# Kernel tuning notes

Hardware: AMD Instinct MI355X
Metric: run time of the kernel (lower is better)

The kernel has to match this reference:

```python
import jax, jax.numpy as jnp
import numpy as np

B = 16          # scene pairs
SRC_N = 512     # src nodes per pair (constant in this setup; reference handles ragged)
REF_N = 512
N_SRC = B * SRC_N
N_REF = B * REF_N
N_TOT = N_SRC + N_REF   # 16384 objects total
P = 128                 # points per object
FEAT = 256              # SGNet node-feature dim / output dim
EMB = 100               # emb_dim
PT_OUT = 256            # pt_out_dim


def setup_inputs() -> dict:
    key = jax.random.key(0)
    ks = jax.random.split(key, 20)
    s = lambda k, *sh: jax.random.normal(k, sh, dtype=jnp.float32) * 0.05
    inp = {
        'tot_obj_pts': jax.random.normal(ks[0], (N_TOT, P, 3), dtype=jnp.float32),
        'src_node_feat': jax.random.normal(ks[1], (N_SRC, FEAT), dtype=jnp.float32),
        'ref_node_feat': jax.random.normal(ks[2], (N_REF, FEAT), dtype=jnp.float32),
        'graph_per_obj_count': jnp.full((B, 2), SRC_N, dtype=jnp.int64),
        'overlap': jax.random.uniform(ks[3], (B,), dtype=jnp.float32),
        'target': jax.random.randint(ks[4], (N_TOT,), 0, 2, dtype=jnp.int64),
        # SGNet (per-node MLP 256 -> 256 -> 256)
        'sg_w1': s(ks[5], FEAT, FEAT), 'sg_b1': jnp.zeros((FEAT,), jnp.float32),
        'sg_w2': s(ks[6], FEAT, FEAT), 'sg_b2': jnp.zeros((FEAT,), jnp.float32),
        # structure_embedding Linear(256, 100)
        'se_w': s(ks[7], FEAT, EMB), 'se_b': jnp.zeros((EMB,), jnp.float32),
        # PointNetfeat 1x1 convs: 3 -> 64 -> 128 -> 256, global max pool
        'p_w1': s(ks[8], 3, 64),    'p_b1': jnp.zeros((64,), jnp.float32),
        'p_w2': s(ks[9], 64, 128),  'p_b2': jnp.zeros((128,), jnp.float32),
        'p_w3': s(ks[10], 128, PT_OUT), 'p_b3': jnp.zeros((PT_OUT,), jnp.float32),
        # object_embedding Linear(256, 100)
        'oe_w': s(ks[11], PT_OUT, EMB), 'oe_b': jnp.zeros((EMB,), jnp.float32),
    }
    return inp


def _interleave_positions(counts):
    """Output positions reproducing the per-pair cat([src_i, ref_i]) ordering."""
    src_c = counts[:, 0]
    ref_c = counts[:, 1]
    excl = lambda c: jnp.concatenate([jnp.zeros((1,), c.dtype), jnp.cumsum(c)[:-1]])
    src_starts = excl(src_c)
    ref_starts = excl(ref_c)
    out_starts = excl(src_c + ref_c)
    b = counts.shape[0]
    b_src = jnp.repeat(jnp.arange(b), src_c, total_repeat_length=N_SRC)
    b_ref = jnp.repeat(jnp.arange(b), ref_c, total_repeat_length=N_REF)
    pos_src = out_starts[b_src] + (jnp.arange(N_SRC) - src_starts[b_src])
    pos_ref = out_starts[b_ref] + src_c[b_ref] + (jnp.arange(N_REF) - ref_starts[b_ref])
    return pos_src, pos_ref


def reference(tot_obj_pts, src_node_feat, ref_node_feat, graph_per_obj_count,
              overlap, target, sg_w1, sg_b1, sg_w2, sg_b2, se_w, se_b,
              p_w1, p_b1, p_w2, p_b2, p_w3, p_b3, oe_w, oe_b):
    # ---- sgnet branch: per-node MLP, then ragged interleave per scene pair ----
    sgnet = lambda x: jax.nn.relu(x @ sg_w1 + sg_b1) @ sg_w2 + sg_b2
    src_emb = sgnet(src_node_feat)   # [N_SRC, 256]
    ref_emb = sgnet(ref_node_feat)   # [N_REF, 256]
    pos_src, pos_ref = _interleave_positions(graph_per_obj_count)
    structure = jnp.zeros((N_TOT, FEAT), src_emb.dtype)
    structure = structure.at[pos_src].set(src_emb).at[pos_ref].set(ref_emb)
    sg_out = structure @ se_w + se_b          # [N_TOT, 100]

    # ---- point branch: PointNet 1x1-conv stack + global max pool ----
    # tot_obj_pts.permute(0,2,1): [N, P, 3] -> per-point linears via einsum
    h = jax.nn.relu(jnp.einsum('npc,cd->npd', tot_obj_pts, p_w1) + p_b1)
    h = jax.nn.relu(jnp.einsum('npc,cd->npd', h, p_w2) + p_b2)
    h = jnp.einsum('npc,cd->npd', h, p_w3) + p_b3   # [N, P, 256]
    feat = jnp.max(h, axis=1)                        # global max over points
    pt_out = feat @ oe_w + oe_b                      # [N_TOT, 100]

    # ---- joint embedding: cat along feature dim ----
    joint = jnp.concatenate([sg_out, pt_out], axis=1)  # [N_TOT, 200]
    return joint
```

## Files before the change

### kernel.cpp

```cpp
#include <hip/hip_runtime.h>
#include <hip/hip_bf16.h>
#include <math.h>

#define B_SZ   16
#define SRC_N  512
#define N_TOT  16384
#define P_PTS  128
#define FEAT   256
#define EMB    100
#define OUT_C  200

typedef __attribute__((ext_vector_type(8))) short short8;
typedef __attribute__((ext_vector_type(8))) unsigned short ushort8;
typedef __attribute__((ext_vector_type(4))) float floatx4;

__device__ __forceinline__ unsigned short f2bf(float x) {
    union { float f; unsigned u; } v; v.f = x;
    unsigned r = v.u + 0x7fffu + ((v.u >> 16) & 1u);
    return (unsigned short)(r >> 16);
}
__device__ __forceinline__ unsigned pack_rne(float a, float b) {
    union { float f; unsigned u; } x, y; x.f = a; y.f = b;
    unsigned lo = x.u + 0x7fffu + ((x.u >> 16) & 1u);
    unsigned hi = y.u + 0x7fffu + ((y.u >> 16) & 1u);
    return __builtin_amdgcn_perm(hi, lo, 0x07060302);
}
__device__ __forceinline__ unsigned pack_rhu(float a, float b) {
    union { float f; unsigned u; } x, y; x.f = a; y.f = b;
    return __builtin_amdgcn_perm(y.u + 0x8000u, x.u + 0x8000u, 0x07060302);
}

#define WS_PW2T 0
#define WS_PW3T 8192
#define WS_POET 40960
#define WS_SGW1 66560
#define WS_SGW2 132096
#define WS_SGSE 197632
#define WS_TOT  226304

__device__ __forceinline__ int perm32(int p) {
    return 32 * (p >> 5) + 16 * (p & 1) + ((p >> 1) & 15);
}

__global__ void prep_kernel(const float* __restrict__ pw2,
                            const float* __restrict__ pw3,
                            const float* __restrict__ oew,
                            const float* __restrict__ sw1,
                            const float* __restrict__ sw2,
                            const float* __restrict__ sew,
                            unsigned short* __restrict__ ws) {
    const int o = blockIdx.x * 256 + threadIdx.x;
    if (o < WS_PW3T) {
        const int n = o >> 6, k = o & 63;
        ws[o] = f2bf(pw2[k * 128 + n]);
    } else if (o < WS_POET) {
        const int i = o - WS_PW3T;
        const int n = i >> 7, k = i & 127;
        ws[o] = f2bf(pw3[k * 256 + n]);
    } else if (o < WS_SGW1) {
        const int i = o - WS_POET;
        const int j = i >> 8, c = i & 255;
        ws[o] = f2bf(oew[c * EMB + j]);
    } else if (o < WS_SGW2) {
        const int i = o - WS_SGW1;
        const int n = i >> 8, k = i & 255;
        ws[o] = f2bf(sw1[k * 256 + n]);
    } else if (o < WS_SGSE) {
        const int i = o - WS_SGW2;
        const int n = i >> 8, kp = i & 255;
        ws[o] = f2bf(sw2[perm32(kp) * 256 + n]);
    } else if (o < WS_TOT) {
        const int i = o - WS_SGSE;
        const int n = i >> 8, kp = i & 255;
        ws[o] = (n < EMB) ? f2bf(sew[perm32(kp) * EMB + n]) : (unsigned short)0;
    }
}

#define SXS 264

template <bool RELU>
__device__ __forceinline__ void sg_layer(const unsigned short* s_in,
                                         unsigned short* s_out,
                                         const unsigned short* wT,
                                         const float* __restrict__ bias,
                                         int wave, int lm, int lq) {
#pragma unroll
    for (int np = 0; np < 2; np++) {
        short8 bf[2][8];
        float bv[2];
#pragma unroll
        for (int b = 0; b < 2; b++) {
            const int n = wave * 64 + (2 * np + b) * 16 + lm;
            bv[b] = bias[n];
#pragma unroll
            for (int kc = 0; kc < 8; kc++)
                bf[b][kc] = *(const short8*)&wT[n * 256 + kc * 32 + lq * 8];
        }
        floatx4 acc[2][2];
#pragma unroll
        for (int b = 0; b < 2; b++)
#pragma unroll
            for (int mt = 0; mt < 2; mt++) acc[b][mt] = {0.f, 0.f, 0.f, 0.f};
#pragma unroll
        for (int mt = 0; mt < 2; mt++) {
            short8 af[8];
#pragma unroll
            for (int kc = 0; kc < 8; kc++)
                af[kc] = *(const short8*)&s_in[(mt * 16 + lm) * SXS + kc * 32 + lq * 8];
#pragma unroll
            for (int b = 0; b < 2; b++)
#pragma unroll
                for (int kc = 0; kc < 8; kc++)
                    acc[b][mt] = __builtin_amdgcn_mfma_f32_16x16x32_bf16(
                        af[kc], bf[b][kc], acc[b][mt], 0, 0, 0);
        }
#pragma unroll
        for (int mt = 0; mt < 2; mt++)
#pragma unroll
            for (int r = 0; r < 4; r++) {
                float v0 = acc[0][mt][r] + bv[0];
                float v1 = acc[1][mt][r] + bv[1];
                if (RELU) { v0 = fmaxf(v0, 0.f); v1 = fmaxf(v1, 0.f); }
                *(unsigned*)&s_out[(mt * 16 + lq * 4 + r) * SXS +
                                   wave * 64 + 32 * np + 2 * lm] = pack_rne(v0, v1);
            }
    }
}

__global__ __launch_bounds__(256, 2) void sgnet_mfma_kernel(
    const float* __restrict__ src_feat, const float* __restrict__ ref_feat,
    const float* __restrict__ b1, const float* __restrict__ b2,
    const float* __restrict__ seb, const unsigned short* __restrict__ ws,
    float* __restrict__ out)
{
    __shared__ __align__(16) unsigned short s_x[32 * SXS];
    __shared__ __align__(16) unsigned short s_h[32 * SXS];

    const unsigned short* w1T = ws + WS_SGW1;
    const unsigned short* w2T = ws + WS_SGW2;
    const unsigned short* seT = ws + WS_SGSE;

    const int blk = blockIdx.x;
    const bool is_ref = (blk >= 256);
    const int row0 = (blk & 255) * 32;
    const float* feat = is_ref ? ref_feat : src_feat;
    const int t = threadIdx.x;
    const int wave = t >> 6, lane = t & 63, lm = lane & 15, lq = lane >> 4;

#pragma unroll
    for (int i = 0; i < 4; i++) {
        const int flat = i * 2048 + t * 8;
        const int r = flat >> 8, c = flat & 255;
        const float4 a = *(const float4*)&feat[(row0 + r) * 256 + c];
        const float4 b = *(const float4*)&feat[(row0 + r) * 256 + c + 4];
        uint4 d;
        d.x = pack_rne(a.x, a.y); d.y = pack_rne(a.z, a.w);
        d.z = pack_rne(b.x, b.y); d.w = pack_rne(b.z, b.w);
        *(uint4*)&s_x[r * SXS + c] = d;
    }
    __syncthreads();

    sg_layer<true>(s_x, s_h, w1T, b1, wave, lm, lq);
    __syncthreads();
    sg_layer<false>(s_h, s_x, w2T, b2, wave, lm, lq);
    __syncthreads();

#pragma unroll
    for (int s = 0; s < 2; s++) {
        const int ntt = wave * 2 + s;
        if (ntt >= 7) continue;
        const int j = ntt * 16 + lm;
        short8 bf[8];
#pragma unroll
        for (int kc = 0; kc < 8; kc++)
            bf[kc] = *(const short8*)&seT[j * 256 + kc * 32 + lq * 8];
        const float bj = (j < EMB) ? seb[j] : 0.f;
#pragma unroll
        for (int mt = 0; mt < 2; mt++) {
            short8 af[8];
#pragma unroll
            for (int kc = 0; kc < 8; kc++)
                af[kc] = *(const short8*)&s_x[(mt * 16 + lm) * SXS + kc * 32 + lq * 8];
            floatx4 acc = {0.f, 0.f, 0.f, 0.f};
#pragma unroll
            for (int kc = 0; kc < 8; kc++)
                acc = __builtin_amdgcn_mfma_f32_16x16x32_bf16(af[kc], bf[kc], acc, 0, 0, 0);
            if (j < EMB) {
#pragma unroll
                for (int r = 0; r < 4; r++) {
                    const int grow = row0 + mt * 16 + lq * 4 + r;
                    const int pos = ((grow >> 9) << 10) + (grow & 511) + (is_ref ? 512 : 0);
                    out[pos * OUT_C + j] = acc[r] + bj;
                }
            }
        }
    }
}

#define H1S 72
#define H2S 136

__global__ __launch_bounds__(256, 3) void pointnet_mfma_kernel(
    const float* __restrict__ pts,
    const float* __restrict__ w1, const float* __restrict__ b1,
    const float* __restrict__ b2, const float* __restrict__ b3,
    const unsigned short* __restrict__ ws,
    const float* __restrict__ oeb, float* __restrict__ out)
{
    __shared__ __align__(16) unsigned short s_h1[128 * H1S];
    __shared__ __align__(16) unsigned short s_h2[128 * H2S];
    float* s_pts  = (float*)s_h2;
    float* s_tmp  = (float*)s_h1;
    float* s_feat = (float*)s_h1 + 16 * 264;

    const unsigned short* w2T = ws + WS_PW2T;
    const unsigned short* w3T = ws + WS_PW3T;
    const unsigned short* oeT = ws + WS_POET;

    const int obj  = blockIdx.x;
    const int t    = threadIdx.x;
    const int wave = t >> 6, lane = t & 63, lm = lane & 15, lq = lane >> 4;

    short8 w2f[2][2];
    float4 b2v[2];
#pragma unroll
    for (int mi = 0; mi < 2; mi++) {
        const int m = (wave * 2 + mi) * 16 + lm;
#pragma unroll
        for (int kc = 0; kc < 2; kc++)
            w2f[mi][kc] = *(const short8*)&w2T[m * 64 + kc * 32 + lq * 8];
        b2v[mi] = *(const float4*)&b2[(wave * 2 + mi) * 16 + lq * 4];
    }

    for (int i = t; i < P_PTS * 3; i += 256)
        s_pts[i] = pts[obj * (P_PTS * 3) + i];
    __syncthreads();

    {
        const int k0 = (t & 7) * 8;
        float wr0[8], wr1[8], wr2[8], br[8];
#pragma unroll
        for (int j = 0; j < 8; j++) {
            wr0[j] = w1[k0 + j]; wr1[j] = w1[64 + k0 + j];
            wr2[j] = w1[128 + k0 + j]; br[j] = b1[k0 + j];
        }
#pragma unroll
        for (int i = 0; i < 4; i++) {
            const int m = (t >> 3) + i * 32;
            const float x = s_pts[m * 3 + 0];
            const float y = s_pts[m * 3 + 1];
            const float z = s_pts[m * 3 + 2];
            float v[8];
#pragma unroll
            for (int j = 0; j < 8; j++)
                v[j] = fmaxf(br[j] + x * wr0[j] + y * wr1[j] + z * wr2[j], 0.f);
            uint4 d;
            d.x = pack_rhu(v[0], v[1]); d.y = pack_rhu(v[2], v[3]);
            d.z = pack_rhu(v[4], v[5]); d.w = pack_rhu(v[6], v[7]);
            *(uint4*)&s_h1[m * H1S + k0] = d;
        }
    }

    short8 w3f[4][4];
#pragma unroll
    for (int mi = 0; mi < 4; mi++) {
        const int m = (wave * 4 + mi) * 16 + lm;
#pragma unroll
        for (int kc = 0; kc < 4; kc++)
            w3f[mi][kc] = *(const short8*)&w3T[m * 128 + kc * 32 + lq * 8];
    }
    __syncthreads();

#pragma unroll
    for (int nt = 0; nt < 8; nt++) {
        short8 hf[2];
#pragma unroll
        for (int kc = 0; kc < 2; kc++)
            hf[kc] = *(const short8*)&s_h1[(nt * 16 + lm) * H1S + kc * 32 + lq * 8];
#pragma unroll
        for (int mi = 0; mi < 2; mi++) {
            floatx4 acc = {0.f, 0.f, 0.f, 0.f};
            acc = __builtin_amdgcn_mfma_f32_16x16x32_bf16(w2f[mi][0], hf[0], acc, 0, 0, 0);
            acc = __builtin_amdgcn_mfma_f32_16x16x32_bf16(w2f[mi][1], hf[1], acc, 0, 0, 0);
            const float v0 = fmaxf(acc[0] + b2v[mi].x, 0.f);
            const float v1 = fmaxf(acc[1] + b2v[mi].y, 0.f);
            const float v2 = fmaxf(acc[2] + b2v[mi].z, 0.f);
            const float v3 = fmaxf(acc[3] + b2v[mi].w, 0.f);
            uint2 dd;
            dd.x = pack_rhu(v0, v1);
            dd.y = pack_rhu(v2, v3);
            *(uint2*)&s_h2[(nt * 16 + lm) * H2S + (wave * 2 + mi) * 16 + lq * 4] = dd;
        }
    }
    __syncthreads();

    {
        floatx4 mx[4];
#pragma unroll
        for (int mi = 0; mi < 4; mi++) mx[mi] = {-1e30f, -1e30f, -1e30f, -1e30f};
#pragma unroll
        for (int nt = 0; nt < 8; nt++) {
            short8 hf[4];
#pragma unroll
            for (int kc = 0; kc < 4; kc++)
                hf[kc] = *(const short8*)&s_h2[(nt * 16 + lm) * H2S + kc * 32 + lq * 8];
#pragma unroll
            for (int mi = 0; mi < 4; mi++) {
                floatx4 acc = {0.f, 0.f, 0.f, 0.f};
#pragma unroll
                for (int kc = 0; kc < 4; kc++)
                    acc = __builtin_amdgcn_mfma_f32_16x16x32_bf16(w3f[mi][kc], hf[kc], acc, 0, 0, 0);
#pragma unroll
                for (int r = 0; r < 4; r++)
                    mx[mi][r] = fmaxf(mx[mi][r], acc[r]);
            }
        }
#pragma unroll
        for (int mi = 0; mi < 4; mi++)
            *(floatx4*)&s_tmp[lm * 264 + (wave * 4 + mi) * 16 + lq * 4] = mx[mi];
    }
    __syncthreads();

    {
        float m = s_tmp[t];
#pragma unroll
        for (int l = 1; l < 16; l++) m = fmaxf(m, s_tmp[l * 264 + t]);
        s_feat[t] = m + b3[t];
    }
    __syncthreads();

    if (t < 2 * EMB) {
        const int j = t >> 1, half = t & 1;
        float acc = half ? 0.f : oeb[j];
        const unsigned short* orow = &oeT[j * 256 + half * 128];
        const float* f = &s_feat[half * 128];
        for (int c8 = 0; c8 < 16; c8++) {
            const ushort8 w8 = *(const ushort8*)&orow[c8 * 8];
            const float4 f0 = *(const float4*)&f[c8 * 8];
            const float4 f1 = *(const float4*)&f[c8 * 8 + 4];
            union { unsigned u; float fl; } cv;
            float s = 0.f;
            cv.u = (unsigned)w8[0] << 16; s += f0.x * cv.fl;
            cv.u = (unsigned)w8[1] << 16; s += f0.y * cv.fl;
            cv.u = (unsigned)w8[2] << 16; s += f0.z * cv.fl;
            cv.u = (unsigned)w8[3] << 16; s += f0.w * cv.fl;
            cv.u = (unsigned)w8[4] << 16; s += f1.x * cv.fl;
            cv.u = (unsigned)w8[5] << 16; s += f1.y * cv.fl;
            cv.u = (unsigned)w8[6] << 16; s += f1.z * cv.fl;
            cv.u = (unsigned)w8[7] << 16; s += f1.w * cv.fl;
            acc += s;
        }
        acc += __shfl_xor(acc, 1, 64);
        if (half == 0) out[obj * OUT_C + EMB + j] = acc;
    }
}

extern "C" void kernel_launch(void* const* d_in, const int* in_sizes, int n_in,
                              void* d_out, int out_size, void* d_ws, size_t ws_size,
                              hipStream_t stream) {
    (void)in_sizes; (void)n_in; (void)out_size; (void)ws_size;
    const float* tot_pts  = (const float*)d_in[0];
    const float* src_feat = (const float*)d_in[1];
    const float* ref_feat = (const float*)d_in[2];
    const float* sg_w1 = (const float*)d_in[6];
    const float* sg_b1 = (const float*)d_in[7];
    const float* sg_w2 = (const float*)d_in[8];
    const float* sg_b2 = (const float*)d_in[9];
    const float* se_w  = (const float*)d_in[10];
    const float* se_b  = (const float*)d_in[11];
    const float* p_w1  = (const float*)d_in[12];
    const float* p_b1  = (const float*)d_in[13];
    const float* p_w2  = (const float*)d_in[14];
    const float* p_b2  = (const float*)d_in[15];
    const float* p_w3  = (const float*)d_in[16];
    const float* p_b3  = (const float*)d_in[17];
    const float* oe_w  = (const float*)d_in[18];
    const float* oe_b  = (const float*)d_in[19];
    float* out = (float*)d_out;
    unsigned short* ws = (unsigned short*)d_ws;

    prep_kernel<<<(WS_TOT + 255) / 256, 256, 0, stream>>>(
        p_w2, p_w3, oe_w, sg_w1, sg_w2, se_w, ws);
    sgnet_mfma_kernel<<<512, 256, 0, stream>>>(src_feat, ref_feat, sg_b1, sg_b2,
                                               se_b, ws, out);
    pointnet_mfma_kernel<<<N_TOT, 256, 0, stream>>>(tot_pts, p_w1, p_b1,
                                                    p_b2, p_b3, ws, oe_b, out);
}
```

Baseline: 416.2 us.

## Fuse SGNet and PointNet into one launch and halve PointNet h2 buffer

```diff
diff --git a/kernel.cpp b/kernel.cpp
--- a/kernel.cpp
+++ b/kernel.cpp
@@ -77,6 +77,9 @@
 }
 
 #define SXS 264
+#define H1S 72
+#define H2S 136
+#define SMEM_BYTES 35840
 
 template <bool RELU>
 __device__ __forceinline__ void sg_layer(const unsigned short* s_in,
@@ -127,20 +130,22 @@
     }
 }
 
-__global__ __launch_bounds__(256, 2) void sgnet_mfma_kernel(
-    const float* __restrict__ src_feat, const float* __restrict__ ref_feat,
-    const float* __restrict__ b1, const float* __restrict__ b2,
-    const float* __restrict__ seb, const unsigned short* __restrict__ ws,
-    float* __restrict__ out)
+__device__ void sgnet_body(unsigned char* smem, int blk,
+                           const float* __restrict__ src_feat,
+                           const float* __restrict__ ref_feat,
+                           const float* __restrict__ b1,
+                           const float* __restrict__ b2,
+                           const float* __restrict__ seb,
+                           const unsigned short* __restrict__ ws,
+                           float* __restrict__ out)
 {
-    __shared__ __align__(16) unsigned short s_x[32 * SXS];
-    __shared__ __align__(16) unsigned short s_h[32 * SXS];
+    unsigned short* s_x = (unsigned short*)smem;
+    unsigned short* s_h = s_x + 32 * SXS;
 
     const unsigned short* w1T = ws + WS_SGW1;
     const unsigned short* w2T = ws + WS_SGW2;
     const unsigned short* seT = ws + WS_SGSE;
 
-    const int blk = blockIdx.x;
     const bool is_ref = (blk >= 256);
     const int row0 = (blk & 255) * 32;
     const float* feat = is_ref ? ref_feat : src_feat;
@@ -197,18 +202,18 @@
     }
 }
 
-#define H1S 72
-#define H2S 136
-
-__global__ __launch_bounds__(256, 3) void pointnet_mfma_kernel(
-    const float* __restrict__ pts,
-    const float* __restrict__ w1, const float* __restrict__ b1,
-    const float* __restrict__ b2, const float* __restrict__ b3,
-    const unsigned short* __restrict__ ws,
-    const float* __restrict__ oeb, float* __restrict__ out)
+__device__ void pointnet_body(unsigned char* smem, int obj,
+                              const float* __restrict__ pts,
+                              const float* __restrict__ w1,
+                              const float* __restrict__ b1,
+                              const float* __restrict__ b2,
+                              const float* __restrict__ b3,
+                              const unsigned short* __restrict__ ws,
+                              const float* __restrict__ oeb,
+                              float* __restrict__ out)
 {
-    __shared__ __align__(16) unsigned short s_h1[128 * H1S];
-    __shared__ __align__(16) unsigned short s_h2[128 * H2S];
+    unsigned short* s_h1 = (unsigned short*)smem;
+    unsigned short* s_h2 = (unsigned short*)(smem + 18432);
     float* s_pts  = (float*)s_h2;
     float* s_tmp  = (float*)s_h1;
     float* s_feat = (float*)s_h1 + 16 * 264;
@@ -217,8 +222,7 @@
     const unsigned short* w3T = ws + WS_PW3T;
     const unsigned short* oeT = ws + WS_POET;
 
-    const int obj  = blockIdx.x;
-    const int t    = threadIdx.x;
+    const int t = threadIdx.x;
     const int wave = t >> 6, lane = t & 63, lm = lane & 15, lq = lane >> 4;
 
     short8 w2f[2][2];
@@ -269,37 +273,39 @@
         for (int kc = 0; kc < 4; kc++)
             w3f[mi][kc] = *(const short8*)&w3T[m * 128 + kc * 32 + lq * 8];
     }
-    __syncthreads();
-
-#pragma unroll
-    for (int nt = 0; nt < 8; nt++) {
-        short8 hf[2];
-#pragma unroll
-        for (int kc = 0; kc < 2; kc++)
-            hf[kc] = *(const short8*)&s_h1[(nt * 16 + lm) * H1S + kc * 32 + lq * 8];
-#pragma unroll
-        for (int mi = 0; mi < 2; mi++) {
-            floatx4 acc = {0.f, 0.f, 0.f, 0.f};
-            acc = __builtin_amdgcn_mfma_f32_16x16x32_bf16(w2f[mi][0], hf[0], acc, 0, 0, 0);
-            acc = __builtin_amdgcn_mfma_f32_16x16x32_bf16(w2f[mi][1], hf[1], acc, 0, 0, 0);
-            const float v0 = fmaxf(acc[0] + b2v[mi].x, 0.f);
-            const float v1 = fmaxf(acc[1] + b2v[mi].y, 0.f);
-            const float v2 = fmaxf(acc[2] + b2v[mi].z, 0.f);
-            const float v3 = fmaxf(acc[3] + b2v[mi].w, 0.f);
-            uint2 dd;
-            dd.x = pack_rhu(v0, v1);
-            dd.y = pack_rhu(v2, v3);
-            *(uint2*)&s_h2[(nt * 16 + lm) * H2S + (wave * 2 + mi) * 16 + lq * 4] = dd;
-        }
-    }
-    __syncthreads();
-
-    {
-        floatx4 mx[4];
-#pragma unroll
-        for (int mi = 0; mi < 4; mi++) mx[mi] = {-1e30f, -1e30f, -1e30f, -1e30f};
-#pragma unroll
-        for (int nt = 0; nt < 8; nt++) {
+
+    floatx4 mx[4];
+#pragma unroll
+    for (int mi = 0; mi < 4; mi++) mx[mi] = {-1e30f, -1e30f, -1e30f, -1e30f};
+
+    __syncthreads();
+
+    for (int c = 0; c < 2; c++) {
+#pragma unroll
+        for (int nt = 0; nt < 4; nt++) {
+            short8 hf[2];
+#pragma unroll
+            for (int kc = 0; kc < 2; kc++)
+                hf[kc] = *(const short8*)&s_h1[(c * 64 + nt * 16 + lm) * H1S + kc * 32 + lq * 8];
+#pragma unroll
+            for (int mi = 0; mi < 2; mi++) {
+                floatx4 acc = {0.f, 0.f, 0.f, 0.f};
+                acc = __builtin_amdgcn_mfma_f32_16x16x32_bf16(w2f[mi][0], hf[0], acc, 0, 0, 0);
+                acc = __builtin_amdgcn_mfma_f32_16x16x32_bf16(w2f[mi][1], hf[1], acc, 0, 0, 0);
+                const float v0 = fmaxf(acc[0] + b2v[mi].x, 0.f);
+                const float v1 = fmaxf(acc[1] + b2v[mi].y, 0.f);
+                const float v2 = fmaxf(acc[2] + b2v[mi].z, 0.f);
+                const float v3 = fmaxf(acc[3] + b2v[mi].w, 0.f);
+                uint2 dd;
+                dd.x = pack_rhu(v0, v1);
+                dd.y = pack_rhu(v2, v3);
+                *(uint2*)&s_h2[(nt * 16 + lm) * H2S + (wave * 2 + mi) * 16 + lq * 4] = dd;
+            }
+        }
+        __syncthreads();
+
+#pragma unroll
+        for (int nt = 0; nt < 4; nt++) {
             short8 hf[4];
 #pragma unroll
             for (int kc = 0; kc < 4; kc++)
@@ -315,10 +321,12 @@
                     mx[mi][r] = fmaxf(mx[mi][r], acc[r]);
             }
         }
-#pragma unroll
-        for (int mi = 0; mi < 4; mi++)
-            *(floatx4*)&s_tmp[lm * 264 + (wave * 4 + mi) * 16 + lq * 4] = mx[mi];
-    }
+        __syncthreads();
+    }
+
+#pragma unroll
+    for (int mi = 0; mi < 4; mi++)
+        *(floatx4*)&s_tmp[lm * 264 + (wave * 4 + mi) * 16 + lq * 4] = mx[mi];
     __syncthreads();
 
     {
@@ -352,6 +360,26 @@
         }
         acc += __shfl_xor(acc, 1, 64);
         if (half == 0) out[obj * OUT_C + EMB + j] = acc;
+    }
+}
+
+__global__ __launch_bounds__(256, 4) void fused_kernel(
+    const float* __restrict__ pts,
+    const float* __restrict__ src_feat, const float* __restrict__ ref_feat,
+    const float* __restrict__ sg_b1, const float* __restrict__ sg_b2,
+    const float* __restrict__ seb,
+    const float* __restrict__ p_w1, const float* __restrict__ p_b1,
+    const float* __restrict__ p_b2, const float* __restrict__ p_b3,
+    const float* __restrict__ oeb,
+    const unsigned short* __restrict__ ws,
+    float* __restrict__ out)
+{
+    __shared__ __align__(16) unsigned char smem[SMEM_BYTES];
+    const int blk = blockIdx.x;
+    if (blk < 512) {
+        sgnet_body(smem, blk, src_feat, ref_feat, sg_b1, sg_b2, seb, ws, out);
+    } else {
+        pointnet_body(smem, blk - 512, pts, p_w1, p_b1, p_b2, p_b3, ws, oeb, out);
     }
 }
 
@@ -381,8 +409,7 @@
 
     prep_kernel<<<(WS_TOT + 255) / 256, 256, 0, stream>>>(
         p_w2, p_w3, oe_w, sg_w1, sg_w2, se_w, ws);
-    sgnet_mfma_kernel<<<512, 256, 0, stream>>>(src_feat, ref_feat, sg_b1, sg_b2,
-                                               se_b, ws, out);
-    pointnet_mfma_kernel<<<N_TOT, 256, 0, stream>>>(tot_pts, p_w1, p_b1,
-                                                    p_b2, p_b3, ws, oe_b, out);
-}
+    fused_kernel<<<512 + N_TOT, 256, 0, stream>>>(
+        tot_pts, src_feat, ref_feat, sg_b1, sg_b2, se_b,
+        p_w1, p_b1, p_b2, p_b3, oe_b, ws, out);
+}
```

Result: slower. 567.4 us (+36.3%).

## Widen PointNet blocks to 512 threads and halve SGNet row tiles

Applied to the files above, without the earlier changes.

```diff
diff --git a/kernel.cpp b/kernel.cpp
--- a/kernel.cpp
+++ b/kernel.cpp
@@ -77,6 +77,8 @@
 }
 
 #define SXS 264
+#define H1S 72
+#define H2S 136
 
 template <bool RELU>
 __device__ __forceinline__ void sg_layer(const unsigned short* s_in,
@@ -96,59 +98,52 @@
             for (int kc = 0; kc < 8; kc++)
                 bf[b][kc] = *(const short8*)&wT[n * 256 + kc * 32 + lq * 8];
         }
-        floatx4 acc[2][2];
+        short8 af[8];
+#pragma unroll
+        for (int kc = 0; kc < 8; kc++)
+            af[kc] = *(const short8*)&s_in[lm * SXS + kc * 32 + lq * 8];
+        floatx4 acc[2];
+#pragma unroll
+        for (int b = 0; b < 2; b++) acc[b] = {0.f, 0.f, 0.f, 0.f};
 #pragma unroll
         for (int b = 0; b < 2; b++)
 #pragma unroll
-            for (int mt = 0; mt < 2; mt++) acc[b][mt] = {0.f, 0.f, 0.f, 0.f};
-#pragma unroll
-        for (int mt = 0; mt < 2; mt++) {
-            short8 af[8];
-#pragma unroll
             for (int kc = 0; kc < 8; kc++)
-                af[kc] = *(const short8*)&s_in[(mt * 16 + lm) * SXS + kc * 32 + lq * 8];
-#pragma unroll
-            for (int b = 0; b < 2; b++)
-#pragma unroll
-                for (int kc = 0; kc < 8; kc++)
-                    acc[b][mt] = __builtin_amdgcn_mfma_f32_16x16x32_bf16(
-                        af[kc], bf[b][kc], acc[b][mt], 0, 0, 0);
-        }
-#pragma unroll
-        for (int mt = 0; mt < 2; mt++)
-#pragma unroll
-            for (int r = 0; r < 4; r++) {
-                float v0 = acc[0][mt][r] + bv[0];
-                float v1 = acc[1][mt][r] + bv[1];
-                if (RELU) { v0 = fmaxf(v0, 0.f); v1 = fmaxf(v1, 0.f); }
-                *(unsigned*)&s_out[(mt * 16 + lq * 4 + r) * SXS +
-                                   wave * 64 + 32 * np + 2 * lm] = pack_rne(v0, v1);
-            }
-    }
-}
-
-__global__ __launch_bounds__(256, 2) void sgnet_mfma_kernel(
+                acc[b] = __builtin_amdgcn_mfma_f32_16x16x32_bf16(
+                    af[kc], bf[b][kc], acc[b], 0, 0, 0);
+#pragma unroll
+        for (int r = 0; r < 4; r++) {
+            float v0 = acc[0][r] + bv[0];
+            float v1 = acc[1][r] + bv[1];
+            if (RELU) { v0 = fmaxf(v0, 0.f); v1 = fmaxf(v1, 0.f); }
+            *(unsigned*)&s_out[(lq * 4 + r) * SXS +
+                               wave * 64 + 32 * np + 2 * lm] = pack_rne(v0, v1);
+        }
+    }
+}
+
+__global__ __launch_bounds__(256, 3) void sgnet_mfma_kernel(
     const float* __restrict__ src_feat, const float* __restrict__ ref_feat,
     const float* __restrict__ b1, const float* __restrict__ b2,
     const float* __restrict__ seb, const unsigned short* __restrict__ ws,
     float* __restrict__ out)
 {
-    __shared__ __align__(16) unsigned short s_x[32 * SXS];
-    __shared__ __align__(16) unsigned short s_h[32 * SXS];
+    __shared__ __align__(16) unsigned short s_x[16 * SXS];
+    __shared__ __align__(16) unsigned short s_h[16 * SXS];
 
     const unsigned short* w1T = ws + WS_SGW1;
     const unsigned short* w2T = ws + WS_SGW2;
     const unsigned short* seT = ws + WS_SGSE;
 
     const int blk = blockIdx.x;
-    const bool is_ref = (blk >= 256);
-    const int row0 = (blk & 255) * 32;
+    const bool is_ref = (blk >= 512);
+    const int row0 = (blk & 511) * 16;
     const float* feat = is_ref ? ref_feat : src_feat;
     const int t = threadIdx.x;
     const int wave = t >> 6, lane = t & 63, lm = lane & 15, lq = lane >> 4;
 
 #pragma unroll
-    for (int i = 0; i < 4; i++) {
+    for (int i = 0; i < 2; i++) {
         const int flat = i * 2048 + t * 8;
         const int r = flat >> 8, c = flat & 255;
         const float4 a = *(const float4*)&feat[(row0 + r) * 256 + c];
@@ -175,32 +170,26 @@
         for (int kc = 0; kc < 8; kc++)
             bf[kc] = *(const short8*)&seT[j * 256 + kc * 32 + lq * 8];
         const float bj = (j < EMB) ? seb[j] : 0.f;
-#pragma unroll
-        for (int mt = 0; mt < 2; mt++) {
-            short8 af[8];
-#pragma unroll
-            for (int kc = 0; kc < 8; kc++)
-                af[kc] = *(const short8*)&s_x[(mt * 16 + lm) * SXS + kc * 32 + lq * 8];
-            floatx4 acc = {0.f, 0.f, 0.f, 0.f};
-#pragma unroll
-            for (int kc = 0; kc < 8; kc++)
-                acc = __builtin_amdgcn_mfma_f32_16x16x32_bf16(af[kc], bf[kc], acc, 0, 0, 0);
-            if (j < EMB) {
-#pragma unroll
-                for (int r = 0; r < 4; r++) {
-                    const int grow = row0 + mt * 16 + lq * 4 + r;
-                    const int pos = ((grow >> 9) << 10) + (grow & 511) + (is_ref ? 512 : 0);
-                    out[pos * OUT_C + j] = acc[r] + bj;
-                }
+        short8 af[8];
+#pragma unroll
+        for (int kc = 0; kc < 8; kc++)
+            af[kc] = *(const short8*)&s_x[lm * SXS + kc * 32 + lq * 8];
+        floatx4 acc = {0.f, 0.f, 0.f, 0.f};
+#pragma unroll
+        for (int kc = 0; kc < 8; kc++)
+            acc = __builtin_amdgcn_mfma_f32_16x16x32_bf16(af[kc], bf[kc], acc, 0, 0, 0);
+        if (j < EMB) {
+#pragma unroll
+            for (int r = 0; r < 4; r++) {
+                const int grow = row0 + lq * 4 + r;
+                const int pos = ((grow >> 9) << 10) + (grow & 511) + (is_ref ? 512 : 0);
+                out[pos * OUT_C + j] = acc[r] + bj;
             }
         }
     }
 }
 
-#define H1S 72
-#define H2S 136
-
-__global__ __launch_bounds__(256, 3) void pointnet_mfma_kernel(
+__global__ __launch_bounds__(512, 4) void pointnet_mfma_kernel(
     const float* __restrict__ pts,
     const float* __restrict__ w1, const float* __restrict__ b1,
     const float* __restrict__ b2, const float* __restrict__ b3,
@@ -208,7 +197,7 @@
     const float* __restrict__ oeb, float* __restrict__ out)
 {
     __shared__ __align__(16) unsigned short s_h1[128 * H1S];
-    __shared__ __align__(16) unsigned short s_h2[128 * H2S];
+    __shared__ __align__(16) unsigned short s_h2[64 * H2S];
     float* s_pts  = (float*)s_h2;
     float* s_tmp  = (float*)s_h1;
     float* s_feat = (float*)s_h1 + 16 * 264;
@@ -221,19 +210,13 @@
     const int t    = threadIdx.x;
     const int wave = t >> 6, lane = t & 63, lm = lane & 15, lq = lane >> 4;
 
-    short8 w2f[2][2];
-    float4 b2v[2];
-#pragma unroll
-    for (int mi = 0; mi < 2; mi++) {
-        const int m = (wave * 2 + mi) * 16 + lm;
-#pragma unroll
-        for (int kc = 0; kc < 2; kc++)
-            w2f[mi][kc] = *(const short8*)&w2T[m * 64 + kc * 32 + lq * 8];
-        b2v[mi] = *(const float4*)&b2[(wave * 2 + mi) * 16 + lq * 4];
-    }
-
-    for (int i = t; i < P_PTS * 3; i += 256)
-        s_pts[i] = pts[obj * (P_PTS * 3) + i];
+    short8 w2f[2];
+#pragma unroll
+    for (int kc = 0; kc < 2; kc++)
+        w2f[kc] = *(const short8*)&w2T[(wave * 16 + lm) * 64 + kc * 32 + lq * 8];
+    const float4 b2v = *(const float4*)&b2[wave * 16 + lq * 4];
+
+    if (t < P_PTS * 3) s_pts[t] = pts[obj * (P_PTS * 3) + t];
     __syncthreads();
 
     {
@@ -245,8 +228,8 @@
             wr2[j] = w1[128 + k0 + j]; br[j] = b1[k0 + j];
         }
 #pragma unroll
-        for (int i = 0; i < 4; i++) {
-            const int m = (t >> 3) + i * 32;
+        for (int i = 0; i < 2; i++) {
+            const int m = (t >> 3) + i * 64;
             const float x = s_pts[m * 3 + 0];
             const float y = s_pts[m * 3 + 1];
             const float z = s_pts[m * 3 + 2];
@@ -261,51 +244,50 @@
         }
     }
 
-    short8 w3f[4][4];
-#pragma unroll
-    for (int mi = 0; mi < 4; mi++) {
-        const int m = (wave * 4 + mi) * 16 + lm;
+    short8 w3f[2][4];
+#pragma unroll
+    for (int mi = 0; mi < 2; mi++) {
+        const int m = (wave * 2 + mi) * 16 + lm;
 #pragma unroll
         for (int kc = 0; kc < 4; kc++)
             w3f[mi][kc] = *(const short8*)&w3T[m * 128 + kc * 32 + lq * 8];
     }
-    __syncthreads();
-
-#pragma unroll
-    for (int nt = 0; nt < 8; nt++) {
-        short8 hf[2];
-#pragma unroll
-        for (int kc = 0; kc < 2; kc++)
-            hf[kc] = *(const short8*)&s_h1[(nt * 16 + lm) * H1S + kc * 32 + lq * 8];
-#pragma unroll
-        for (int mi = 0; mi < 2; mi++) {
+
+    floatx4 mx[2];
+#pragma unroll
+    for (int mi = 0; mi < 2; mi++) mx[mi] = {-1e30f, -1e30f, -1e30f, -1e30f};
+
+    __syncthreads();
+
+    for (int c = 0; c < 2; c++) {
+#pragma unroll
+        for (int nt = 0; nt < 4; nt++) {
+            short8 hf[2];
+#pragma unroll
+            for (int kc = 0; kc < 2; kc++)
+                hf[kc] = *(const short8*)&s_h1[(c * 64 + nt * 16 + lm) * H1S + kc * 32 + lq * 8];
             floatx4 acc = {0.f, 0.f, 0.f, 0.f};
-            acc = __builtin_amdgcn_mfma_f32_16x16x32_bf16(w2f[mi][0], hf[0], acc, 0, 0, 0);
-            acc = __builtin_amdgcn_mfma_f32_16x16x32_bf16(w2f[mi][1], hf[1], acc, 0, 0, 0);
-            const float v0 = fmaxf(acc[0] + b2v[mi].x, 0.f);
-            const float v1 = fmaxf(acc[1] + b2v[mi].y, 0.f);
-            const float v2 = fmaxf(acc[2] + b2v[mi].z, 0.f);
-            const float v3 = fmaxf(acc[3] + b2v[mi].w, 0.f);
+            acc = __builtin_amdgcn_mfma_f32_16x16x32_bf16(w2f[0], hf[0], acc, 0, 0, 0);
+            acc = __builtin_amdgcn_mfma_f32_16x16x32_bf16(w2f[1], hf[1], acc, 0, 0, 0);
+            const float v0 = fmaxf(acc[0] + b2v.x, 0.f);
+            const float v1 = fmaxf(acc[1] + b2v.y, 0.f);
+            const float v2 = fmaxf(acc[2] + b2v.z, 0.f);
+            const float v3 = fmaxf(acc[3] + b2v.w, 0.f);
             uint2 dd;
             dd.x = pack_rhu(v0, v1);
             dd.y = pack_rhu(v2, v3);
-            *(uint2*)&s_h2[(nt * 16 + lm) * H2S + (wave * 2 + mi) * 16 + lq * 4] = dd;
-        }
-    }
-    __syncthreads();
-
-    {
-        floatx4 mx[4];
-#pragma unroll
-        for (int mi = 0; mi < 4; mi++) mx[mi] = {-1e30f, -1e30f, -1e30f, -1e30f};
-#pragma unroll
-        for (int nt = 0; nt < 8; nt++) {
+            *(uint2*)&s_h2[(nt * 16 + lm) * H2S + wave * 16 + lq * 4] = dd;
+        }
+        __syncthreads();
+
+#pragma unroll
+        for (int nt = 0; nt < 4; nt++) {
             short8 hf[4];
 #pragma unroll
             for (int kc = 0; kc < 4; kc++)
                 hf[kc] = *(const short8*)&s_h2[(nt * 16 + lm) * H2S + kc * 32 + lq * 8];
 #pragma unroll
-            for (int mi = 0; mi < 4; mi++) {
+            for (int mi = 0; mi < 2; mi++) {
                 floatx4 acc = {0.f, 0.f, 0.f, 0.f};
 #pragma unroll
                 for (int kc = 0; kc < 4; kc++)
@@ -315,13 +297,15 @@
                     mx[mi][r] = fmaxf(mx[mi][r], acc[r]);
             }
         }
-#pragma unroll
-        for (int mi = 0; mi < 4; mi++)
-            *(floatx4*)&s_tmp[lm * 264 + (wave * 4 + mi) * 16 + lq * 4] = mx[mi];
-    }
-    __syncthreads();
-
-    {
+        __syncthreads();
+    }
+
+#pragma unroll
+    for (int mi = 0; mi < 2; mi++)
+        *(floatx4*)&s_tmp[lm * 264 + (wave * 2 + mi) * 16 + lq * 4] = mx[mi];
+    __syncthreads();
+
+    if (t < 256) {
         float m = s_tmp[t];
 #pragma unroll
         for (int l = 1; l < 16; l++) m = fmaxf(m, s_tmp[l * 264 + t]);
@@ -329,12 +313,12 @@
     }
     __syncthreads();
 
-    if (t < 2 * EMB) {
-        const int j = t >> 1, half = t & 1;
-        float acc = half ? 0.f : oeb[j];
-        const unsigned short* orow = &oeT[j * 256 + half * 128];
-        const float* f = &s_feat[half * 128];
-        for (int c8 = 0; c8 < 16; c8++) {
+    if (t < 4 * EMB) {
+        const int j = t >> 2, q = t & 3;
+        float acc = (q == 0) ? oeb[j] : 0.f;
+        const unsigned short* orow = &oeT[j * 256 + q * 64];
+        const float* f = &s_feat[q * 64];
+        for (int c8 = 0; c8 < 8; c8++) {
             const ushort8 w8 = *(const ushort8*)&orow[c8 * 8];
             const float4 f0 = *(const float4*)&f[c8 * 8];
             const float4 f1 = *(const float4*)&f[c8 * 8 + 4];
@@ -351,7 +335,8 @@
             acc += s;
         }
         acc += __shfl_xor(acc, 1, 64);
-        if (half == 0) out[obj * OUT_C + EMB + j] = acc;
+        acc += __shfl_xor(acc, 2, 64);
+        if (q == 0) out[obj * OUT_C + EMB + j] = acc;
     }
 }
 
@@ -381,8 +366,8 @@
 
     prep_kernel<<<(WS_TOT + 255) / 256, 256, 0, stream>>>(
         p_w2, p_w3, oe_w, sg_w1, sg_w2, se_w, ws);
-    sgnet_mfma_kernel<<<512, 256, 0, stream>>>(src_feat, ref_feat, sg_b1, sg_b2,
-                                               se_b, ws, out);
-    pointnet_mfma_kernel<<<N_TOT, 256, 0, stream>>>(tot_pts, p_w1, p_b1,
+    sgnet_mfma_kernel<<<1024, 256, 0, stream>>>(src_feat, ref_feat, sg_b1, sg_b2,
+                                                se_b, ws, out);
+    pointnet_mfma_kernel<<<N_TOT, 512, 0, stream>>>(tot_pts, p_w1, p_b1,
                                                     p_b2, p_b3, ws, oe_b, out);
 }
```

New measurement: 455.4 us. 9.4% more time.
